# Kernel tuning notes

Hardware: AMD Instinct MI355X
Metric: run time of the kernel (lower is better)

## Reference

```python
import jax, jax.numpy as jnp
import numpy as np

H, N, CH, RANK = 512, 64, 1, 1
SEQ_L = 4096


def setup_inputs() -> dict:
    key = jax.random.key(0)
    k0, k1, k2, k3, k4 = jax.random.split(key, 5)
    # A = -exp(A_real) + i*A_imag  (real_transform='exp'); HiPPO-style imag init
    A_real = jnp.log(0.5 + jax.random.uniform(k0, (H, N), dtype=jnp.float32))
    A_imag = jnp.broadcast_to(np.pi * jnp.arange(N, dtype=jnp.float32), (H, N)).copy()
    # complex params stored as (..., 2) real/imag pairs (torch.view_as_real layout)
    B = (0.5 ** 0.5) * jax.random.normal(k1, (1, H, N, 2), dtype=jnp.float32)
    C = jax.random.normal(k2, (CH, H, N, 2), dtype=jnp.float32)
    P = (0.5 ** 0.5) * jax.random.normal(k3, (RANK, H, N, 2), dtype=jnp.float32)
    # dt = exp(inv_dt) log-uniform in [1e-3, 1e-1]  (dt_transform='exp')
    lo, hi = np.log(1e-3), np.log(1e-1)
    inv_dt = (lo + (hi - lo) * jax.random.uniform(k4, (H,), dtype=jnp.float32)).astype(jnp.float32)
    return {"A_real": A_real, "A_imag": A_imag, "B": B, "C": C, "P": P,
            "inv_dt": inv_dt, "L": SEQ_L}


def _c(x):
    # view_as_complex
    return x[..., 0] + 1j * x[..., 1]


def _s4_kernel(A_real, A_imag, B, C, P, inv_dt, L):
    dt = jnp.exp(inv_dt)                       # (H,)
    A = -jnp.exp(A_real) + 1j * A_imag          # (H, N) complex64
    Bc, Cc, Pc = _c(B), _c(C), _c(P)            # (1,H,N), (CH,H,N), (R,H,N)
    Q = jnp.conj(Pc)

    Lf = L // 2 + 1
    omega = jnp.exp(-2j * jnp.pi / L) ** jnp.arange(Lf)   # FFT nodes, (Lf,)
    z = 2 * (1 - omega) / (1 + omega)                      # bilinear-transform freqs

    A_dt = A * dt[:, None]                     # (H, N)
    Bcat = jnp.concatenate([Bc, Pc], axis=0)   # (1+R, H, N)
    Ccat = jnp.concatenate([Cc, Q], axis=0)    # (CH+R, H, N)
    v = Bcat[:, None] * Ccat[None]             # (1+R, CH+R, H, N)
    v = v * dt[:, None]

    # Cauchy kernel with implicit conjugate-pair symmetry:
    #   r[a,b,h,l] = sum_n v/(z - A_dt) + conj(v)/(z - conj(A_dt))
    denom = 1.0 / (z - A_dt[..., None])                    # (H, N, Lf)
    r = jnp.einsum('abhn,hnl->abhl', v, denom)
    denom_c = 1.0 / (z - jnp.conj(A_dt)[..., None])
    r = r + jnp.einsum('abhn,hnl->abhl', jnp.conj(v), denom_c)

    # rank-1 Woodbury correction
    k_f = r[:-1, :-1] - r[:-1, -1:] * r[-1:, :-1] / (1 + r[-1:, -1:])
    k_f = k_f * 2 / (1 + omega)

    k = jnp.fft.irfft(k_f, n=L)                # (1, CH, H, L) real
    k = k[..., :L]
    return k[-1]                               # k_B: (CH, H, L)


def reference(A_real, A_imag, B, C, P, inv_dt, L):
    return _s4_kernel(A_real, A_imag, B, C, P, inv_dt, L)
```

## Files before the change

kernel.cpp:

```cpp
#include <hip/hip_runtime.h>
#include <math.h>

namespace {
constexpr int kH = 512;
constexpr int kN = 64;
constexpr int kL = 4096;
constexpr int kM = 2048;
constexpr int kPairRec = 40;
constexpr int kThreads = 512;
constexpr float kPi = 3.14159265358979323846f;
}

typedef float v2f __attribute__((ext_vector_type(2)));

__device__ __forceinline__ int lpad(int i) { return i + (i >> 4); }
__device__ __forceinline__ v2f fma2(v2f a, v2f b, v2f c) {
    return __builtin_elementwise_fma(a, b, c);
}
__device__ __forceinline__ float2 cmul(float2 a, float2 b) {
    return make_float2(a.x*b.x - a.y*b.y, a.x*b.y + a.y*b.x);
}

__global__ __launch_bounds__(kThreads, 4)
void s4_all(const float* __restrict__ A_real, const float* __restrict__ A_imag,
            const float* __restrict__ Bv, const float* __restrict__ Cv,
            const float* __restrict__ Pv, const float* __restrict__ inv_dt,
            float* __restrict__ out)
{
    __shared__ v2f    CREC[(kN/2) * kPairRec / 2];
    __shared__ float  sNyq;
    __shared__ float2 XS[kM];
    __shared__ float2 W2[kM + kM / 16];
    __shared__ float2 TW[kM / 2 + kM / 32];

    const int h   = blockIdx.x;
    const int tid = threadIdx.x;

    for (int j = tid; j < kM / 2; j += kThreads) {
        float s, c;
        sincosf((2.0f * kPi / (float)kM) * (float)j, &s, &c);
        TW[lpad(j)] = make_float2(c, s);
    }

    if (tid < kN) {
        const int n = tid;
        const int idx = h * kN + n;
        const float dt = expf(inv_dt[h]);
        const float ar = -expf(A_real[idx]) * dt;
        const float ai =  A_imag[idx] * dt;
        const float br = Bv[idx*2+0], bi = Bv[idx*2+1];
        const float cr = Cv[idx*2+0], ci = Cv[idx*2+1];
        const float pr = Pv[idx*2+0], pi = Pv[idx*2+1];
        const float v00r = (br*cr - bi*ci)*dt, v00i = (br*ci + bi*cr)*dt;
        const float v01r = (br*pr + bi*pi)*dt, v01i = (bi*pr - br*pi)*dt;
        const float v10r = (pr*cr - pi*ci)*dt, v10i = (pr*ci + pi*cr)*dt;
        const float v11r = (pr*pr + pi*pi)*dt;
        const float ar2 = ar*ar;
        const float C1  = ar2 + ai*ai;
        const float dd  = ar2 - ai*ai;

        float co[16];
        co[0]  = -2.f*C1*(v00r*ar + v00i*ai);   co[1]  = 2.f*(v00i*ai - v00r*ar);
        co[2]  = -4.f*v00r*dd - 8.f*v00i*ar*ai; co[3]  = -4.f*v00r;
        co[4]  = -2.f*C1*(v01r*ar + v01i*ai);   co[5]  = 2.f*(v01i*ai - v01r*ar);
        co[6]  = -4.f*v01r*dd - 8.f*v01i*ar*ai; co[7]  = -4.f*v01r;
        co[8]  = -2.f*C1*(v10r*ar + v10i*ai);   co[9]  = 2.f*(v10i*ai - v10r*ar);
        co[10] = -4.f*v10r*dd - 8.f*v10i*ar*ai; co[11] = -4.f*v10r;
        co[12] = -2.f*C1*(v11r*ar);             co[13] = -2.f*v11r*ar;
        co[14] = -4.f*v11r*dd;                  co[15] = -4.f*v11r;

        float* base = (float*)CREC + (size_t)(n >> 1) * kPairRec + (n & 1);
        base[0] = ai;
        base[2] = ar2;
        #pragma unroll
        for (int k = 0; k < 16; ++k) base[4 + 2*k] = co[k];

        float s = v00r;
        #pragma unroll
        for (int off = 32; off > 0; off >>= 1) s += __shfl_down(s, off, 64);
        if (n == 0) sNyq = s;
    }
    __syncthreads();

    #pragma unroll 1
    for (int pass = 0; pass < 2; ++pass) {
        const int la = pass * 1024 + tid;

        float tvb[2];
        v2f t2p[2], spv[2];
        #pragma unroll
        for (int bb = 0; bb < 2; ++bb) {
            const int l = la + 512 * bb;
            float sn, cn;
            sincosf((float)l * (kPi / (float)kL), &sn, &cn);
            tvb[bb] = sn / cn;
            const float t2 = 2.f * tvb[bb];
            const float sv = t2 * t2;
            t2p[bb] = (v2f){t2, t2};
            spv[bb] = (v2f){sv, sv};
        }

        v2f accR[2][4], accI[2][4];
        #pragma unroll
        for (int bb = 0; bb < 2; ++bb)
            #pragma unroll
            for (int p = 0; p < 4; ++p) {
                accR[bb][p] = (v2f){0.f, 0.f};
                accI[bb][p] = (v2f){0.f, 0.f};
            }

        #pragma unroll 2
        for (int j = 0; j < kN/2; ++j) {
            const v2f* r = CREC + j * (kPairRec/2);
            const v2f aip  = r[0];
            const v2f ar2p = r[1];
            #pragma unroll
            for (int bb = 0; bb < 2; ++bb) {
                const v2f w1 = t2p[bb] - aip;
                const v2f w2 = t2p[bb] + aip;
                const v2f m1 = fma2(w1, w1, ar2p);
                const v2f m2 = fma2(w2, w2, ar2p);
                const v2f D  = m1 * m2;
                const float qq = __builtin_amdgcn_rcpf(D.x * D.y);
                v2f qv;
                qv.x = D.y * qq;
                qv.y = D.x * qq;
                #pragma unroll
                for (int p = 0; p < 4; ++p) {
                    const v2f tr = fma2(spv[bb], r[2 + 4*p + 1], r[2 + 4*p + 0]);
                    const v2f ti = fma2(spv[bb], r[2 + 4*p + 3], r[2 + 4*p + 2]);
                    accR[bb][p] = fma2(tr, qv, accR[bb][p]);
                    accI[bb][p] = fma2(ti, qv, accI[bb][p]);
                }
            }
        }

        #pragma unroll
        for (int bb = 0; bb < 2; ++bb) {
            const int l = la + 512 * bb;
            const float t = tvb[bb];
            const float s00r = accR[bb][0].x + accR[bb][0].y;
            const float s00i = t * (accI[bb][0].x + accI[bb][0].y);
            const float s01r = accR[bb][1].x + accR[bb][1].y;
            const float s01i = t * (accI[bb][1].x + accI[bb][1].y);
            const float s10r = accR[bb][2].x + accR[bb][2].y;
            const float s10i = t * (accI[bb][2].x + accI[bb][2].y);
            const float s11r = accR[bb][3].x + accR[bb][3].y;
            const float s11i = t * (accI[bb][3].x + accI[bb][3].y);
            const float nr = s01r*s10r - s01i*s10i;
            const float ni = s01r*s10i + s01i*s10r;
            const float dr = 1.f + s11r, di = s11i;
            const float qd = __builtin_amdgcn_rcpf(fmaf(dr, dr, di*di));
            const float wr = (nr*dr + ni*di) * qd;
            const float wi = (ni*dr - nr*di) * qd;
            const float gr = s00r - wr, gi = s00i - wi;
            XS[l] = make_float2(fmaf(-gi, t, gr), fmaf(gr, t, gi));
        }
    }
    __syncthreads();

    const float nyqR = sNyq;
    for (int k = tid; k <= kM / 2; k += kThreads) {
        const float2 Xa = XS[k];
        const float2 Xb = (k == 0) ? make_float2(nyqR, 0.0f) : XS[kM - k];
        const float Er = 0.5f * (Xa.x + Xb.x);
        const float Ei = 0.5f * (Xa.y - Xb.y);
        const float Dr = 0.5f * (Xa.x - Xb.x);
        const float Di = 0.5f * (Xa.y + Xb.y);
        float s, c;
        sincosf((2.0f * kPi / (float)kL) * (float)k, &s, &c);
        const float Or = c * Dr - s * Di;
        const float Oi = c * Di + s * Dr;
        const int rk = (int)(__brev((unsigned)k) >> 21);
        W2[lpad(rk)] = make_float2(Er - Oi, Ei + Or);
        if (k != 0 && k != kM / 2) {
            const int rmk = (int)(__brev((unsigned)(kM - k)) >> 21);
            W2[lpad(rmk)] = make_float2(Er + Oi, Or - Ei);
        }
    }
    __syncthreads();

    for (int j = tid; j < kM / 4; j += kThreads) {
        const int i0 = j * 4;
        const float2 e0 = W2[lpad(i0)];
        const float2 e1 = W2[lpad(i0 + 1)];
        const float2 e2 = W2[lpad(i0 + 2)];
        const float2 e3 = W2[lpad(i0 + 3)];
        const float2 a0 = make_float2(e0.x + e1.x, e0.y + e1.y);
        const float2 a1 = make_float2(e0.x - e1.x, e0.y - e1.y);
        const float2 a2 = make_float2(e2.x + e3.x, e2.y + e3.y);
        const float2 a3 = make_float2(e2.x - e3.x, e2.y - e3.y);
        W2[lpad(i0)]     = make_float2(a0.x + a2.x, a0.y + a2.y);
        W2[lpad(i0 + 2)] = make_float2(a0.x - a2.x, a0.y - a2.y);
        W2[lpad(i0 + 1)] = make_float2(a1.x - a3.y, a1.y + a3.x);
        W2[lpad(i0 + 3)] = make_float2(a1.x + a3.y, a1.y - a3.x);
    }
    __syncthreads();

    #pragma unroll
    for (int lg = 2; lg <= 8; lg += 2) {
        const int hs = 1 << lg;
        const int twstride = 512 >> lg;
        for (int j = tid; j < kM / 4; j += kThreads) {
            const int pos = j & (hs - 1);
            const int grp = j >> lg;
            const int i0  = grp * 4 * hs + pos;
            const float2 e0 = W2[lpad(i0)];
            const float2 e1 = W2[lpad(i0 + hs)];
            const float2 e2 = W2[lpad(i0 + 2*hs)];
            const float2 e3 = W2[lpad(i0 + 3*hs)];
            const float2 wB = TW[lpad(pos * twstride)];
            const float2 wA = cmul(wB, wB);
            const float2 t1 = cmul(wA, e1);
            const float2 t3 = cmul(wA, e3);
            const float2 a0 = make_float2(e0.x + t1.x, e0.y + t1.y);
            const float2 a1 = make_float2(e0.x - t1.x, e0.y - t1.y);
            const float2 a2 = make_float2(e2.x + t3.x, e2.y + t3.y);
            const float2 a3 = make_float2(e2.x - t3.x, e2.y - t3.y);
            const float2 u2 = cmul(wB, a2);
            const float2 u3 = cmul(wB, a3);
            W2[lpad(i0)]        = make_float2(a0.x + u2.x, a0.y + u2.y);
            W2[lpad(i0 + 2*hs)] = make_float2(a0.x - u2.x, a0.y - u2.y);
            W2[lpad(i0 + hs)]   = make_float2(a1.x - u3.y, a1.y + u3.x);
            W2[lpad(i0 + 3*hs)] = make_float2(a1.x + u3.y, a1.y - u3.x);
        }
        __syncthreads();
    }
    for (int j = tid; j < kM / 2; j += kThreads) {
        const float2 tw = TW[lpad(j)];
        const float2 a  = W2[lpad(j)];
        const float2 b  = W2[lpad(j + 1024)];
        const float2 tb = cmul(tw, b);
        W2[lpad(j)]        = make_float2(a.x + tb.x, a.y + tb.y);
        W2[lpad(j + 1024)] = make_float2(a.x - tb.x, a.y - tb.y);
    }
    __syncthreads();

    const float invM = 1.0f / (float)kM;
    float2* out2 = (float2*)(out + (size_t)h * kL);
    for (int n = tid; n < kM; n += kThreads) {
        const float2 zn = W2[lpad(n)];
        out2[n] = make_float2(zn.x * invM, zn.y * invM);
    }
}

extern "C" void kernel_launch(void* const* d_in, const int* in_sizes, int n_in,
                              void* d_out, int out_size, void* d_ws, size_t ws_size,
                              hipStream_t stream) {
    const float* A_real = (const float*)d_in[0];
    const float* A_imag = (const float*)d_in[1];
    const float* B      = (const float*)d_in[2];
    const float* C      = (const float*)d_in[3];
    const float* P      = (const float*)d_in[4];
    const float* inv_dt = (const float*)d_in[5];
    float* out = (float*)d_out;

    s4_all<<<dim3(kH), dim3(kThreads), 0, stream>>>(A_real, A_imag, B, C, P,
                                                    inv_dt, out);
}
```

Measured before the change: 105.5 us.

## Split coefficient prep into separate kernel and read records from global memory

Moves per-head Cauchy coefficient precomputation into a small prep kernel that writes records to workspace. The main kernel then reads them through uniform global/scalar loads instead of LDS, which drops one LDS array and one barrier. The inner loop is also rearranged so the numerator polynomial is folded into the accumulator FMAs via a precomputed spv*qv product. The cost is an extra kernel launch and a global round trip for the coefficients.

```diff
diff --git a/kernel.cpp b/kernel.cpp
--- a/kernel.cpp
+++ b/kernel.cpp
@@ -21,14 +21,55 @@
     return make_float2(a.x*b.x - a.y*b.y, a.x*b.y + a.y*b.x);
 }
 
+__global__ __launch_bounds__(64)
+void s4_prep(const float* __restrict__ A_real, const float* __restrict__ A_imag,
+             const float* __restrict__ Bv, const float* __restrict__ Cv,
+             const float* __restrict__ Pv, const float* __restrict__ inv_dt,
+             float* __restrict__ cst, float* __restrict__ xnyq)
+{
+    const int h = blockIdx.x;
+    const int n = threadIdx.x;
+    const int idx = h * kN + n;
+    const float dt = expf(inv_dt[h]);
+    const float ar = -expf(A_real[idx]) * dt;
+    const float ai =  A_imag[idx] * dt;
+    const float br = Bv[idx*2+0], bi = Bv[idx*2+1];
+    const float cr = Cv[idx*2+0], ci = Cv[idx*2+1];
+    const float pr = Pv[idx*2+0], pi = Pv[idx*2+1];
+    const float v00r = (br*cr - bi*ci)*dt, v00i = (br*ci + bi*cr)*dt;
+    const float v01r = (br*pr + bi*pi)*dt, v01i = (bi*pr - br*pi)*dt;
+    const float v10r = (pr*cr - pi*ci)*dt, v10i = (pr*ci + pi*cr)*dt;
+    const float v11r = (pr*pr + pi*pi)*dt;
+    const float ar2 = ar*ar;
+    const float C1  = ar2 + ai*ai;
+    const float dd  = ar2 - ai*ai;
+
+    float co[16];
+    co[0]  = -2.f*C1*(v00r*ar + v00i*ai);   co[1]  = 2.f*(v00i*ai - v00r*ar);
+    co[2]  = -4.f*v00r*dd - 8.f*v00i*ar*ai; co[3]  = -4.f*v00r;
+    co[4]  = -2.f*C1*(v01r*ar + v01i*ai);   co[5]  = 2.f*(v01i*ai - v01r*ar);
+    co[6]  = -4.f*v01r*dd - 8.f*v01i*ar*ai; co[7]  = -4.f*v01r;
+    co[8]  = -2.f*C1*(v10r*ar + v10i*ai);   co[9]  = 2.f*(v10i*ai - v10r*ar);
+    co[10] = -4.f*v10r*dd - 8.f*v10i*ar*ai; co[11] = -4.f*v10r;
+    co[12] = -2.f*C1*(v11r*ar);             co[13] = -2.f*v11r*ar;
+    co[14] = -4.f*v11r*dd;                  co[15] = -4.f*v11r;
+
+    float* base = cst + ((size_t)h * (kN/2) + (n >> 1)) * kPairRec + (n & 1);
+    base[0] = ai;
+    base[2] = ar2;
+    #pragma unroll
+    for (int k = 0; k < 16; ++k) base[4 + 2*k] = co[k];
+
+    float s = v00r;
+    #pragma unroll
+    for (int off = 32; off > 0; off >>= 1) s += __shfl_down(s, off, 64);
+    if (n == 0) xnyq[h] = s;
+}
+
 __global__ __launch_bounds__(kThreads, 4)
-void s4_all(const float* __restrict__ A_real, const float* __restrict__ A_imag,
-            const float* __restrict__ Bv, const float* __restrict__ Cv,
-            const float* __restrict__ Pv, const float* __restrict__ inv_dt,
-            float* __restrict__ out)
+void s4_spec_ifft(const float* __restrict__ cst, const float* __restrict__ xnyq,
+                  float* __restrict__ out)
 {
-    __shared__ v2f    CREC[(kN/2) * kPairRec / 2];
-    __shared__ float  sNyq;
     __shared__ float2 XS[kM];
     __shared__ float2 W2[kM + kM / 16];
     __shared__ float2 TW[kM / 2 + kM / 32];
@@ -42,46 +83,7 @@
         TW[lpad(j)] = make_float2(c, s);
     }
 
-    if (tid < kN) {
-        const int n = tid;
-        const int idx = h * kN + n;
-        const float dt = expf(inv_dt[h]);
-        const float ar = -expf(A_real[idx]) * dt;
-        const float ai =  A_imag[idx] * dt;
-        const float br = Bv[idx*2+0], bi = Bv[idx*2+1];
-        const float cr = Cv[idx*2+0], ci = Cv[idx*2+1];
-        const float pr = Pv[idx*2+0], pi = Pv[idx*2+1];
-        const float v00r = (br*cr - bi*ci)*dt, v00i = (br*ci + bi*cr)*dt;
-        const float v01r = (br*pr + bi*pi)*dt, v01i = (bi*pr - br*pi)*dt;
-        const float v10r = (pr*cr - pi*ci)*dt, v10i = (pr*ci + pi*cr)*dt;
-        const float v11r = (pr*pr + pi*pi)*dt;
-        const float ar2 = ar*ar;
-        const float C1  = ar2 + ai*ai;
-        const float dd  = ar2 - ai*ai;
-
-        float co[16];
-        co[0]  = -2.f*C1*(v00r*ar + v00i*ai);   co[1]  = 2.f*(v00i*ai - v00r*ar);
-        co[2]  = -4.f*v00r*dd - 8.f*v00i*ar*ai; co[3]  = -4.f*v00r;
-        co[4]  = -2.f*C1*(v01r*ar + v01i*ai);   co[5]  = 2.f*(v01i*ai - v01r*ar);
-        co[6]  = -4.f*v01r*dd - 8.f*v01i*ar*ai; co[7]  = -4.f*v01r;
-        co[8]  = -2.f*C1*(v10r*ar + v10i*ai);   co[9]  = 2.f*(v10i*ai - v10r*ar);
-        co[10] = -4.f*v10r*dd - 8.f*v10i*ar*ai; co[11] = -4.f*v10r;
-        co[12] = -2.f*C1*(v11r*ar);             co[13] = -2.f*v11r*ar;
-        co[14] = -4.f*v11r*dd;                  co[15] = -4.f*v11r;
-
-        float* base = (float*)CREC + (size_t)(n >> 1) * kPairRec + (n & 1);
-        base[0] = ai;
-        base[2] = ar2;
-        #pragma unroll
-        for (int k = 0; k < 16; ++k) base[4 + 2*k] = co[k];
-
-        float s = v00r;
-        #pragma unroll
-        for (int off = 32; off > 0; off >>= 1) s += __shfl_down(s, off, 64);
-        if (n == 0) sNyq = s;
-    }
-    __syncthreads();
-
+    const v2f* rec = (const v2f*)(cst + (size_t)h * (kN/2) * kPairRec);
     #pragma unroll 1
     for (int pass = 0; pass < 2; ++pass) {
         const int la = pass * 1024 + tid;
@@ -111,7 +113,7 @@
 
         #pragma unroll 2
         for (int j = 0; j < kN/2; ++j) {
-            const v2f* r = CREC + j * (kPairRec/2);
+            const v2f* r = rec + j * (kPairRec/2);
             const v2f aip  = r[0];
             const v2f ar2p = r[1];
             #pragma unroll
@@ -125,12 +127,13 @@
                 v2f qv;
                 qv.x = D.y * qq;
                 qv.y = D.x * qq;
+                const v2f sqv = spv[bb] * qv;
                 #pragma unroll
                 for (int p = 0; p < 4; ++p) {
-                    const v2f tr = fma2(spv[bb], r[2 + 4*p + 1], r[2 + 4*p + 0]);
-                    const v2f ti = fma2(spv[bb], r[2 + 4*p + 3], r[2 + 4*p + 2]);
-                    accR[bb][p] = fma2(tr, qv, accR[bb][p]);
-                    accI[bb][p] = fma2(ti, qv, accI[bb][p]);
+                    accR[bb][p] = fma2(r[2 + 4*p + 0], qv,  accR[bb][p]);
+                    accR[bb][p] = fma2(r[2 + 4*p + 1], sqv, accR[bb][p]);
+                    accI[bb][p] = fma2(r[2 + 4*p + 2], qv,  accI[bb][p]);
+                    accI[bb][p] = fma2(r[2 + 4*p + 3], sqv, accI[bb][p]);
                 }
             }
         }
@@ -159,7 +162,7 @@
     }
     __syncthreads();
 
-    const float nyqR = sNyq;
+    const float nyqR = xnyq[h];
     for (int k = tid; k <= kM / 2; k += kThreads) {
         const float2 Xa = XS[k];
         const float2 Xb = (k == 0) ? make_float2(nyqR, 0.0f) : XS[kM - k];
@@ -255,6 +258,10 @@
     const float* inv_dt = (const float*)d_in[5];
     float* out = (float*)d_out;
 
-    s4_all<<<dim3(kH), dim3(kThreads), 0, stream>>>(A_real, A_imag, B, C, P,
-                                                    inv_dt, out);
-}
+    float* cst  = (float*)d_ws;
+    float* xnyq = cst + (size_t)kH * (kN/2) * kPairRec;
+
+    s4_prep<<<dim3(kH), dim3(64), 0, stream>>>(A_real, A_imag, B, C, P, inv_dt,
+                                               cst, xnyq);
+    s4_spec_ifft<<<dim3(kH), dim3(kThreads), 0, stream>>>(cst, xnyq, out);
+}
```

Result: no change. 104.0 us (-1.5%).
